# Performance work log

Hardware: AMD Instinct MI355X
Metric: run time of the kernel (lower is better)

Reference implementation:

```python
import jax, jax.numpy as jnp
import numpy as np
from jax import lax

N_NODES = 150_000
N_EDGES = 1_500_000
N_GRAPHS = 150          # batch_size(30) * sequence_length(5), hardcoded in forward
BATCH_SIZE = 30
SEQ_LEN = 5
IN_F = 1
HID = 100               # gcn_hidden_size == lstm_hidden_size


def setup_inputs() -> dict:
    key = jax.random.key(0)
    ks = jax.random.split(key, 12)
    x = jax.random.normal(ks[0], (N_NODES, IN_F), dtype=jnp.float32)
    edge_index = jax.random.randint(ks[1], (2, N_EDGES), 0, N_NODES, dtype=jnp.int32)
    # 150 graphs of 1000 nodes each (contiguous, as PyG batching produces)
    batch = jnp.repeat(jnp.arange(N_GRAPHS, dtype=jnp.int32), N_NODES // N_GRAPHS)
    s = 0.1
    params = {
        # GCNConv layer 1: Linear(no bias) weight stored [in, out]; separate bias
        "W1": jax.random.normal(ks[2], (IN_F, HID), jnp.float32) * s,
        "b1": jnp.zeros((HID,), jnp.float32),
        # GCNConv layer 2
        "W2": jax.random.normal(ks[3], (HID, HID), jnp.float32) * s,
        "b2": jnp.zeros((HID,), jnp.float32),
        # LSTM (PyTorch gate order i,f,g,o), weights [4H, in]/[4H, H]
        "W_ih": jax.random.normal(ks[4], (4 * HID, HID), jnp.float32) * s,
        "W_hh": jax.random.normal(ks[5], (4 * HID, HID), jnp.float32) * s,
        "b_ih": jnp.zeros((4 * HID,), jnp.float32),
        "b_hh": jnp.zeros((4 * HID,), jnp.float32),
        # output head Linear(HID, 1)
        "W_out": jax.random.normal(ks[6], (1, HID), jnp.float32) * s,
        "b_out": jnp.zeros((1,), jnp.float32),
    }
    return {"x": x, "edge_index": edge_index, "batch": batch, **params}


def _gcn_conv(x, src, dst, W, b, n_nodes):
    """PyG GCNConv: h = W x; out = D^-1/2 (A+I) D^-1/2 h + b."""
    h = x @ W  # [N, HID]
    deg = jax.ops.segment_sum(jnp.ones_like(dst, dtype=h.dtype), dst, num_segments=n_nodes)
    dinv = lax.rsqrt(deg)  # deg >= 1 thanks to self loops
    norm = dinv[src] * dinv[dst]  # [E+N]
    msg = h[src] * norm[:, None]  # gather + scale (memory-bound hot loop)
    out = jax.ops.segment_sum(msg, dst, num_segments=n_nodes)
    return out + b


def _lstm_last_hidden(xs, W_ih, W_hh, b_ih, b_hh):
    """xs: [B, T, H] -> last hidden state [B, H] (single-layer LSTM)."""
    B = xs.shape[0]
    H = W_hh.shape[1]
    h0 = jnp.zeros((B, H), xs.dtype)
    c0 = jnp.zeros((B, H), xs.dtype)

    def step(carry, xt):
        h, c = carry
        gates = xt @ W_ih.T + h @ W_hh.T + (b_ih + b_hh)
        i, f, g, o = jnp.split(gates, 4, axis=-1)
        c = jax.nn.sigmoid(f) * c + jax.nn.sigmoid(i) * jnp.tanh(g)
        h = jax.nn.sigmoid(o) * jnp.tanh(c)
        return (h, c), None

    (h_last, _), _ = lax.scan(step, (h0, c0), jnp.swapaxes(xs, 0, 1))
    return h_last


def reference(x, edge_index, batch, W1, b1, W2, b2, W_ih, W_hh, b_ih, b_hh, W_out, b_out):
    n_nodes = x.shape[0]
    loops = jnp.arange(n_nodes, dtype=edge_index.dtype)
    src = jnp.concatenate([edge_index[0], loops])
    dst = jnp.concatenate([edge_index[1], loops])

    h = _gcn_conv(x, src, dst, W1, b1, n_nodes)
    h = _gcn_conv(h, src, dst, W2, b2, n_nodes)

    # global mean pool over 150 graphs
    sums = jax.ops.segment_sum(h, batch, num_segments=N_GRAPHS)
    cnts = jax.ops.segment_sum(jnp.ones((n_nodes,), h.dtype), batch, num_segments=N_GRAPHS)
    pooled = sums / jnp.maximum(cnts, 1.0)[:, None]  # [150, HID]

    seq = pooled.reshape(BATCH_SIZE, SEQ_LEN, -1)  # [30, 5, HID]
    h_last = _lstm_last_hidden(seq, W_ih, W_hh, b_ih, b_hh)
    prediction = h_last @ W_out.T + b_out  # [30, 1]
    return prediction
```

## Files before the change

kernel.cpp:

```cpp
#include <hip/hip_runtime.h>
#include <math.h>

#define N_NODES   150000
#define N_EDGES   1500000
#define N_GRAPHS  150
#define HID       100
#define BATCH     30
#define SEQ       5
#define NODES_PER_GRAPH 1000

#define NPB       256
#define NB        ((N_NODES + NPB - 1) / NPB)
#define SBLK      512
#define EPB       2932
#define CAP       3584
#define FIFO      16

__global__ __launch_bounds__(256) void k_s1(const int* __restrict__ dst,
                                            int* __restrict__ blockBase) {
    __shared__ int hist[NB];
    int t = threadIdx.x;
    for (int i = t; i < NB; i += 256) hist[i] = 0;
    __syncthreads();
    int base = blockIdx.x * EPB;
    int end  = min(base + EPB, N_EDGES);
    for (int i = base + t * 4; i < end; i += 1024) {
        int4 d = *reinterpret_cast<const int4*>(dst + i);
        atomicAdd(&hist[d.x >> 8], 1);
        atomicAdd(&hist[d.y >> 8], 1);
        atomicAdd(&hist[d.z >> 8], 1);
        atomicAdd(&hist[d.w >> 8], 1);
    }
    __syncthreads();
    for (int j = t; j < NB; j += 256)
        blockBase[blockIdx.x * NB + j] = hist[j];
}

__global__ __launch_bounds__(512) void k_colscan(int* __restrict__ blockBase,
                                                 int* __restrict__ bucketCount,
                                                 float* __restrict__ graphA,
                                                 float* __restrict__ graphW) {
    __shared__ int v[SBLK];
    int j = blockIdx.x;
    int t = threadIdx.x;
    if (t == 0 && j < N_GRAPHS) { graphA[j] = 0.0f; graphW[j] = 0.0f; }
    int val = blockBase[t * NB + j];
    v[t] = val;
    __syncthreads();
    for (int off = 1; off < SBLK; off <<= 1) {
        int w = (t >= off) ? v[t - off] : 0;
        __syncthreads();
        v[t] += w;
        __syncthreads();
    }
    blockBase[t * NB + j] = v[t] - val;
    if (t == SBLK - 1) bucketCount[j] = v[t];
}

__global__ __launch_bounds__(256) void k_s2(const int* __restrict__ src,
                                            const int* __restrict__ dst,
                                            const int* __restrict__ blockBase,
                                            unsigned int* __restrict__ sorted) {
    __shared__ unsigned int fifo[NB][FIFO];
    __shared__ int cnt[NB];
    __shared__ int baseS[NB];
    int t = threadIdx.x;
    const int* bb = blockBase + blockIdx.x * NB;
    for (int i = t; i < NB; i += 256) {
        cnt[i] = 0;
        baseS[i] = i * CAP + bb[i];
    }
    __syncthreads();
    int base = blockIdx.x * EPB;
    int end  = min(base + EPB, N_EDGES);
    for (int i = base + t * 4; i < end; i += 1024) {
        int4 s4 = *reinterpret_cast<const int4*>(src + i);
        int4 d4 = *reinterpret_cast<const int4*>(dst + i);
        int bs[4] = { d4.x >> 8, d4.y >> 8, d4.z >> 8, d4.w >> 8 };
        int sv[4] = { s4.x, s4.y, s4.z, s4.w };
        int dl[4] = { d4.x & 255, d4.y & 255, d4.z & 255, d4.w & 255 };
        #pragma unroll
        for (int k = 0; k < 4; ++k) {
            int b = bs[k];
            unsigned int v = ((unsigned int)sv[k] << 8) | (unsigned int)dl[k];
            int slot = atomicAdd(&cnt[b], 1);
            if (slot < FIFO) fifo[b][slot] = v;
            else sorted[baseS[b] + slot] = v;
        }
    }
    __syncthreads();
    int wave = t >> 6, lane = t & 63;
    for (int j = wave; j < NB; j += 4) {
        int c = min(cnt[j], FIFO);
        if (lane < c) sorted[baseS[j] + lane] = fifo[j][lane];
    }
}

__device__ __forceinline__ void graph_reduce_add(float val, int thresh, int nn,
                                                 int g0, float* red, int t,
                                                 float* __restrict__ gdst) {
    red[t] = (t < thresh) ? val : 0.0f;
    __syncthreads();
    for (int s = 128; s > 0; s >>= 1) {
        if (t < s) red[t] += red[t + s];
        __syncthreads();
    }
    if (t == 0) atomicAdd(&gdst[g0], red[0]);
    __syncthreads();
    red[t] = (t >= thresh) ? val : 0.0f;
    __syncthreads();
    for (int s = 128; s > 0; s >>= 1) {
        if (t < s) red[t] += red[t + s];
        __syncthreads();
    }
    if (t == 0 && thresh < nn) atomicAdd(&gdst[g0 + 1], red[0]);
}

__global__ __launch_bounds__(256) void k_accA(const unsigned int* __restrict__ sorted,
                                              const int* __restrict__ bucketCount,
                                              const float* __restrict__ x,
                                              float* __restrict__ pd,
                                              float* __restrict__ px,
                                              float* __restrict__ graphW) {
    __shared__ int degI[2][NPB];
    __shared__ float red[256];
    int b = blockIdx.x;
    int t = threadIdx.x;
    int n0 = b << 8;
    int nn = min(NPB, N_NODES - n0);
    degI[0][t] = 0; degI[1][t] = 0;
    __syncthreads();
    int e0 = b * CAP, e1 = e0 + bucketCount[b];
    int rep = t & 1;
    int nvec = (e1 - e0) >> 2;
    for (int v = t; v < nvec; v += 256) {
        uint4 u4 = *reinterpret_cast<const uint4*>(sorted + e0 + v * 4);
        atomicAdd(&degI[rep][u4.x & 255], 1);
        atomicAdd(&degI[rep][u4.y & 255], 1);
        atomicAdd(&degI[rep][u4.z & 255], 1);
        atomicAdd(&degI[rep][u4.w & 255], 1);
    }
    int tail0 = e0 + (nvec << 2);
    if (tail0 + t < e1) atomicAdd(&degI[rep][sorted[tail0 + t] & 255], 1);
    __syncthreads();
    float val = 0.0f;
    if (t < nn) {
        float dv = 1.0f / sqrtf((float)(1 + degI[0][t] + degI[1][t]));
        pd[n0 + t] = dv;
        px[n0 + t] = dv * x[n0 + t];
        val = dv * dv;
    }
    int g0 = n0 / 1000;
    int thresh = (g0 + 1) * 1000 - n0;
    graph_reduce_add(val, thresh, nn, g0, red, t, graphW);
}

__global__ __launch_bounds__(256) void k_accB(const unsigned int* __restrict__ sorted,
                                              const int* __restrict__ bucketCount,
                                              const float* __restrict__ pd,
                                              const float* __restrict__ px,
                                              float2* __restrict__ pa2,
                                              float* __restrict__ graphA) {
    __shared__ float t1[2][NPB];
    __shared__ float red[256];
    int b = blockIdx.x;
    int t = threadIdx.x;
    int n0 = b << 8;
    int nn = min(NPB, N_NODES - n0);
    t1[0][t] = 0.0f; t1[1][t] = 0.0f;
    __syncthreads();
    int e0 = b * CAP, e1 = e0 + bucketCount[b];
    int rep = t & 1;
    int nvec = (e1 - e0) >> 2;
    for (int v = t; v < nvec; v += 256) {
        uint4 u4 = *reinterpret_cast<const uint4*>(sorted + e0 + v * 4);
        float p0 = px[u4.x >> 8];
        float p1 = px[u4.y >> 8];
        float p2 = px[u4.z >> 8];
        float p3 = px[u4.w >> 8];
        atomicAdd(&t1[rep][u4.x & 255], p0);
        atomicAdd(&t1[rep][u4.y & 255], p1);
        atomicAdd(&t1[rep][u4.z & 255], p2);
        atomicAdd(&t1[rep][u4.w & 255], p3);
    }
    int tail0 = e0 + (nvec << 2);
    if (tail0 + t < e1) {
        unsigned int u = sorted[tail0 + t];
        atomicAdd(&t1[rep][u & 255], px[u >> 8]);
    }
    __syncthreads();
    float val = 0.0f;
    if (t < nn) {
        float dv = pd[n0 + t];
        float T1 = t1[0][t] + t1[1][t];
        float agg1 = dv * T1 + dv * px[n0 + t];
        float a1 = dv * agg1;
        pa2[n0 + t] = make_float2(dv, a1);
        val = dv * a1;
    }
    int g0 = n0 / 1000;
    int thresh = (g0 + 1) * 1000 - n0;
    graph_reduce_add(val, thresh, nn, g0, red, t, graphA);
}

__global__ __launch_bounds__(256) void k_accG(const unsigned int* __restrict__ sorted,
                                              const int* __restrict__ bucketCount,
                                              const float* __restrict__ pd,
                                              const float2* __restrict__ pa2,
                                              float* __restrict__ graphA,
                                              float* __restrict__ graphW) {
    __shared__ float dvl[NPB];
    __shared__ float4 red4[256];
    int b = blockIdx.x;
    int t = threadIdx.x;
    int n0 = b << 8;
    int nn = min(NPB, N_NODES - n0);
    dvl[t] = (t < nn) ? pd[n0 + t] : 0.0f;
    __syncthreads();
    int g0 = n0 / 1000;
    int thresh = (g0 + 1) * 1000 - n0;
    float sa0 = 0.f, sa1 = 0.f, sw0 = 0.f, sw1 = 0.f;
    int e0 = b * CAP, e1 = e0 + bucketCount[b];
    auto proc = [&](unsigned int u) {
        int dl = (int)(u & 255);
        float dvd = dvl[dl];
        float2 v = pa2[u >> 8];
        if (dl < thresh) { sw0 += dvd * v.x; sa0 += dvd * v.y; }
        else             { sw1 += dvd * v.x; sa1 += dvd * v.y; }
    };
    int nvec = (e1 - e0) >> 2;
    for (int v = t; v < nvec; v += 256) {
        uint4 u4 = *reinterpret_cast<const uint4*>(sorted + e0 + v * 4);
        proc(u4.x); proc(u4.y); proc(u4.z); proc(u4.w);
    }
    int tail0 = e0 + (nvec << 2);
    if (tail0 + t < e1) proc(sorted[tail0 + t]);
    red4[t] = make_float4(sa0, sa1, sw0, sw1);
    __syncthreads();
    for (int s = 128; s > 0; s >>= 1) {
        if (t < s) {
            red4[t].x += red4[t + s].x; red4[t].y += red4[t + s].y;
            red4[t].z += red4[t + s].z; red4[t].w += red4[t + s].w;
        }
        __syncthreads();
    }
    if (t == 0) {
        atomicAdd(&graphA[g0], red4[0].x);
        atomicAdd(&graphW[g0], red4[0].z);
        if (thresh < nn) {
            atomicAdd(&graphA[g0 + 1], red4[0].y);
            atomicAdd(&graphW[g0 + 1], red4[0].w);
        }
    }
}

__global__ __launch_bounds__(512) void k_tail(const float* __restrict__ graphA,
                                              const float* __restrict__ graphW,
                                              const float* __restrict__ W1,
                                              const float* __restrict__ b1,
                                              const float* __restrict__ W2,
                                              const float* __restrict__ b2,
                                              const float* __restrict__ W_ih,
                                              const float* __restrict__ W_hh,
                                              const float* __restrict__ b_ih,
                                              const float* __restrict__ b_hh,
                                              const float* __restrict__ W_out,
                                              const float* __restrict__ b_out,
                                              float* __restrict__ outp) {
    int b = blockIdx.x;
    int t = threadIdx.x;
    __shared__ float v1[HID], v2[HID];
    __shared__ float xs_l[SEQ][HID];
    __shared__ float Xg_l[SEQ][4 * HID];
    __shared__ float hs[HID], cs[HID], gsb[4 * HID];
    __shared__ float red[512];

    if (t < HID) {
        float a = 0.0f, c = 0.0f;
        for (int k = 0; k < HID; ++k) {
            float w2 = W2[k * HID + t];
            a += W1[k] * w2;
            c += b1[k] * w2;
        }
        v1[t] = a; v2[t] = c;
    }
    __syncthreads();

    if (t < SEQ * HID) {
        int s = t / HID, j = t - s * HID;
        int g = b * SEQ + s;
        float ma = graphA[g] * (1.0f / NODES_PER_GRAPH);
        float mw = graphW[g] * (1.0f / NODES_PER_GRAPH);
        xs_l[s][j] = ma * v1[j] + mw * v2[j] + b2[j];
    }
    __syncthreads();

    float wreg[HID];
    if (t < 4 * HID) {
        const float4* wp = reinterpret_cast<const float4*>(W_ih + t * HID);
        #pragma unroll
        for (int q = 0; q < HID / 4; ++q) {
            float4 w4 = wp[q];
            wreg[4*q+0] = w4.x; wreg[4*q+1] = w4.y; wreg[4*q+2] = w4.z; wreg[4*q+3] = w4.w;
        }
        float bias = b_ih[t] + b_hh[t];
        for (int s = 0; s < SEQ; ++s) {
            float acc = bias;
            #pragma unroll
            for (int k = 0; k < HID; ++k)
                acc += xs_l[s][k] * wreg[k];
            Xg_l[s][t] = acc;
        }
        wp = reinterpret_cast<const float4*>(W_hh + t * HID);
        #pragma unroll
        for (int q = 0; q < HID / 4; ++q) {
            float4 w4 = wp[q];
            wreg[4*q+0] = w4.x; wreg[4*q+1] = w4.y; wreg[4*q+2] = w4.z; wreg[4*q+3] = w4.w;
        }
    }
    if (t < HID) { hs[t] = 0.0f; cs[t] = 0.0f; }
    __syncthreads();

    for (int step = 0; step < SEQ; ++step) {
        if (t < 4 * HID) {
            float acc = Xg_l[step][t];
            #pragma unroll
            for (int k = 0; k < HID; ++k)
                acc += hs[k] * wreg[k];
            gsb[t] = acc;
        }
        __syncthreads();
        if (t < HID) {
            float ig = 1.0f / (1.0f + expf(-gsb[t]));
            float fg = 1.0f / (1.0f + expf(-gsb[HID + t]));
            float gg = tanhf(gsb[2 * HID + t]);
            float og = 1.0f / (1.0f + expf(-gsb[3 * HID + t]));
            float c  = fg * cs[t] + ig * gg;
            cs[t] = c;
            hs[t] = og * tanhf(c);
        }
        __syncthreads();
    }

    float v = (t < HID) ? hs[t] * W_out[t] : 0.0f;
    red[t] = v;
    __syncthreads();
    for (int s = 256; s > 0; s >>= 1) {
        if (t < s) red[t] += red[t + s];
        __syncthreads();
    }
    if (t == 0) outp[b] = red[0] + b_out[0];
}

static inline char* align_up(char* p, size_t a) {
    return (char*)(((uintptr_t)p + (a - 1)) & ~(uintptr_t)(a - 1));
}

extern "C" void kernel_launch(void* const* d_in, const int* in_sizes, int n_in,
                              void* d_out, int out_size, void* d_ws, size_t ws_size,
                              hipStream_t stream) {
    const float* x    = (const float*)d_in[0];
    const int*   ei   = (const int*)d_in[1];
    const int*   srcp = ei;
    const int*   dstp = ei + N_EDGES;
    const float* W1   = (const float*)d_in[3];
    const float* b1   = (const float*)d_in[4];
    const float* W2   = (const float*)d_in[5];
    const float* b2   = (const float*)d_in[6];
    const float* W_ih = (const float*)d_in[7];
    const float* W_hh = (const float*)d_in[8];
    const float* b_ih = (const float*)d_in[9];
    const float* b_hh = (const float*)d_in[10];
    const float* W_out= (const float*)d_in[11];
    const float* b_out= (const float*)d_in[12];
    float* out = (float*)d_out;

    char* w = (char*)d_ws;
    int*  bucketCount = (int*)w;             w = align_up(w + NB * sizeof(int), 64);
    int*  blockBase   = (int*)w;             w = align_up(w + (size_t)SBLK * NB * sizeof(int), 64);
    unsigned int* sorted = (unsigned int*)w; w = align_up(w + (size_t)NB * CAP * sizeof(unsigned int), 64);
    float*  pd   = (float*)w;                w = align_up(w + (size_t)N_NODES * sizeof(float), 64);
    float*  px   = (float*)w;                w = align_up(w + (size_t)N_NODES * sizeof(float), 64);
    float2* pa2  = (float2*)w;               w = align_up(w + (size_t)N_NODES * sizeof(float2), 64);
    float* graphA = (float*)w;               w = align_up(w + N_GRAPHS * sizeof(float), 64);
    float* graphW = (float*)w;               w = align_up(w + N_GRAPHS * sizeof(float), 64);

    k_s1     <<<SBLK, 256, 0, stream>>>(dstp, blockBase);
    k_colscan<<<NB, SBLK, 0, stream>>>(blockBase, bucketCount, graphA, graphW);
    k_s2     <<<SBLK, 256, 0, stream>>>(srcp, dstp, blockBase, sorted);
    k_accA   <<<NB, 256, 0, stream>>>(sorted, bucketCount, x, pd, px, graphW);
    k_accB   <<<NB, 256, 0, stream>>>(sorted, bucketCount, pd, px, pa2, graphA);
    k_accG   <<<NB, 256, 0, stream>>>(sorted, bucketCount, pd, pa2, graphA, graphW);
    k_tail   <<<BATCH, 512, 0, stream>>>(graphA, graphW, W1, b1, W2, b2,
                                         W_ih, W_hh, b_ih, b_hh, W_out, b_out, out);
}
```

Baseline: 91.86 us.

## Fuse bucket sort into one pass with global atomic bases; defer graph reductions

Replaces the three-kernel bucket sort (histogram, column scan, scatter) with a single kernel that stages edges in shared memory, reserves per-bucket space through global atomics on bucketCount, and then scatters. Per-block graph partial sums are now written without atomics and reduced inside the tail kernel, so the global accumulators no longer need zeroing. This cuts two launches and the blockBase round trip through memory, at the cost of a memset and a nondeterministic edge order within each bucket.

```diff
diff --git a/kernel.cpp b/kernel.cpp
--- a/kernel.cpp
+++ b/kernel.cpp
@@ -9,103 +9,66 @@
 #define SEQ       5
 #define NODES_PER_GRAPH 1000
 
-#define NPB       256
-#define NB        ((N_NODES + NPB - 1) / NPB)
-#define SBLK      512
-#define EPB       2932
-#define CAP       3584
-#define FIFO      16
-
-__global__ __launch_bounds__(256) void k_s1(const int* __restrict__ dst,
-                                            int* __restrict__ blockBase) {
+#define NPB   256
+#define NB    586
+#define SBLK  512
+#define EPB   2932
+#define CAP   3584
+
+__global__ __launch_bounds__(256) void k_sort(const int* __restrict__ src,
+                                              const int* __restrict__ dst,
+                                              int* __restrict__ bucketCount,
+                                              unsigned int* __restrict__ sorted) {
+    __shared__ unsigned int   epack[EPB];
+    __shared__ unsigned short ebuck[EPB];
     __shared__ int hist[NB];
+    __shared__ int baseS[NB];
     int t = threadIdx.x;
     for (int i = t; i < NB; i += 256) hist[i] = 0;
-    __syncthreads();
-    int base = blockIdx.x * EPB;
-    int end  = min(base + EPB, N_EDGES);
-    for (int i = base + t * 4; i < end; i += 1024) {
-        int4 d = *reinterpret_cast<const int4*>(dst + i);
-        atomicAdd(&hist[d.x >> 8], 1);
-        atomicAdd(&hist[d.y >> 8], 1);
-        atomicAdd(&hist[d.z >> 8], 1);
-        atomicAdd(&hist[d.w >> 8], 1);
-    }
-    __syncthreads();
-    for (int j = t; j < NB; j += 256)
-        blockBase[blockIdx.x * NB + j] = hist[j];
-}
-
-__global__ __launch_bounds__(512) void k_colscan(int* __restrict__ blockBase,
-                                                 int* __restrict__ bucketCount,
-                                                 float* __restrict__ graphA,
-                                                 float* __restrict__ graphW) {
-    __shared__ int v[SBLK];
-    int j = blockIdx.x;
-    int t = threadIdx.x;
-    if (t == 0 && j < N_GRAPHS) { graphA[j] = 0.0f; graphW[j] = 0.0f; }
-    int val = blockBase[t * NB + j];
-    v[t] = val;
-    __syncthreads();
-    for (int off = 1; off < SBLK; off <<= 1) {
-        int w = (t >= off) ? v[t - off] : 0;
-        __syncthreads();
-        v[t] += w;
-        __syncthreads();
-    }
-    blockBase[t * NB + j] = v[t] - val;
-    if (t == SBLK - 1) bucketCount[j] = v[t];
-}
-
-__global__ __launch_bounds__(256) void k_s2(const int* __restrict__ src,
-                                            const int* __restrict__ dst,
-                                            const int* __restrict__ blockBase,
-                                            unsigned int* __restrict__ sorted) {
-    __shared__ unsigned int fifo[NB][FIFO];
-    __shared__ int cnt[NB];
-    __shared__ int baseS[NB];
-    int t = threadIdx.x;
-    const int* bb = blockBase + blockIdx.x * NB;
-    for (int i = t; i < NB; i += 256) {
-        cnt[i] = 0;
-        baseS[i] = i * CAP + bb[i];
-    }
     __syncthreads();
     int base = blockIdx.x * EPB;
     int end  = min(base + EPB, N_EDGES);
     for (int i = base + t * 4; i < end; i += 1024) {
         int4 s4 = *reinterpret_cast<const int4*>(src + i);
         int4 d4 = *reinterpret_cast<const int4*>(dst + i);
-        int bs[4] = { d4.x >> 8, d4.y >> 8, d4.z >> 8, d4.w >> 8 };
+        int l = i - base;
         int sv[4] = { s4.x, s4.y, s4.z, s4.w };
         int dl[4] = { d4.x & 255, d4.y & 255, d4.z & 255, d4.w & 255 };
+        int bk[4] = { d4.x >> 8, d4.y >> 8, d4.z >> 8, d4.w >> 8 };
         #pragma unroll
         for (int k = 0; k < 4; ++k) {
-            int b = bs[k];
-            unsigned int v = ((unsigned int)sv[k] << 8) | (unsigned int)dl[k];
-            int slot = atomicAdd(&cnt[b], 1);
-            if (slot < FIFO) fifo[b][slot] = v;
-            else sorted[baseS[b] + slot] = v;
-        }
-    }
-    __syncthreads();
-    int wave = t >> 6, lane = t & 63;
-    for (int j = wave; j < NB; j += 4) {
-        int c = min(cnt[j], FIFO);
-        if (lane < c) sorted[baseS[j] + lane] = fifo[j][lane];
-    }
-}
-
-__device__ __forceinline__ void graph_reduce_add(float val, int thresh, int nn,
-                                                 int g0, float* red, int t,
-                                                 float* __restrict__ gdst) {
+            atomicAdd(&hist[bk[k]], 1);
+            epack[l + k] = ((unsigned int)sv[k] << 8) | (unsigned int)dl[k];
+            ebuck[l + k] = (unsigned short)bk[k];
+        }
+    }
+    __syncthreads();
+    for (int j = t; j < NB; j += 256) {
+        int c = hist[j];
+        int gb = (c > 0) ? atomicAdd(&bucketCount[j], c) : 0;
+        baseS[j] = j * CAP + gb;
+    }
+    __syncthreads();
+    for (int j = t; j < NB; j += 256) hist[j] = 0;
+    __syncthreads();
+    int nloc = end - base;
+    for (int l = t; l < nloc; l += 256) {
+        int bk = ebuck[l];
+        int idx = atomicAdd(&hist[bk], 1);
+        sorted[baseS[bk] + idx] = epack[l];
+    }
+}
+
+__device__ __forceinline__ void bin2_reduce_store(float val, int thresh,
+                                                  float* red, int t,
+                                                  float2* __restrict__ outp) {
     red[t] = (t < thresh) ? val : 0.0f;
     __syncthreads();
     for (int s = 128; s > 0; s >>= 1) {
         if (t < s) red[t] += red[t + s];
         __syncthreads();
     }
-    if (t == 0) atomicAdd(&gdst[g0], red[0]);
+    float b0 = red[0];
     __syncthreads();
     red[t] = (t >= thresh) ? val : 0.0f;
     __syncthreads();
@@ -113,7 +76,7 @@
         if (t < s) red[t] += red[t + s];
         __syncthreads();
     }
-    if (t == 0 && thresh < nn) atomicAdd(&gdst[g0 + 1], red[0]);
+    if (t == 0) *outp = make_float2(b0, red[0]);
 }
 
 __global__ __launch_bounds__(256) void k_accA(const unsigned int* __restrict__ sorted,
@@ -121,7 +84,7 @@
                                               const float* __restrict__ x,
                                               float* __restrict__ pd,
                                               float* __restrict__ px,
-                                              float* __restrict__ graphW) {
+                                              float2* __restrict__ pW) {
     __shared__ int degI[2][NPB];
     __shared__ float red[256];
     int b = blockIdx.x;
@@ -152,7 +115,7 @@
     }
     int g0 = n0 / 1000;
     int thresh = (g0 + 1) * 1000 - n0;
-    graph_reduce_add(val, thresh, nn, g0, red, t, graphW);
+    bin2_reduce_store(val, thresh, red, t, &pW[b]);
 }
 
 __global__ __launch_bounds__(256) void k_accB(const unsigned int* __restrict__ sorted,
@@ -160,14 +123,14 @@
                                               const float* __restrict__ pd,
                                               const float* __restrict__ px,
                                               float2* __restrict__ pa2,
-                                              float* __restrict__ graphA) {
-    __shared__ float t1[2][NPB];
+                                              float2* __restrict__ pA) {
+    __shared__ float t1s[2][NPB];
     __shared__ float red[256];
     int b = blockIdx.x;
     int t = threadIdx.x;
     int n0 = b << 8;
     int nn = min(NPB, N_NODES - n0);
-    t1[0][t] = 0.0f; t1[1][t] = 0.0f;
+    t1s[0][t] = 0.0f; t1s[1][t] = 0.0f;
     __syncthreads();
     int e0 = b * CAP, e1 = e0 + bucketCount[b];
     int rep = t & 1;
@@ -178,21 +141,21 @@
         float p1 = px[u4.y >> 8];
         float p2 = px[u4.z >> 8];
         float p3 = px[u4.w >> 8];
-        atomicAdd(&t1[rep][u4.x & 255], p0);
-        atomicAdd(&t1[rep][u4.y & 255], p1);
-        atomicAdd(&t1[rep][u4.z & 255], p2);
-        atomicAdd(&t1[rep][u4.w & 255], p3);
+        atomicAdd(&t1s[rep][u4.x & 255], p0);
+        atomicAdd(&t1s[rep][u4.y & 255], p1);
+        atomicAdd(&t1s[rep][u4.z & 255], p2);
+        atomicAdd(&t1s[rep][u4.w & 255], p3);
     }
     int tail0 = e0 + (nvec << 2);
     if (tail0 + t < e1) {
         unsigned int u = sorted[tail0 + t];
-        atomicAdd(&t1[rep][u & 255], px[u >> 8]);
+        atomicAdd(&t1s[rep][u & 255], px[u >> 8]);
     }
     __syncthreads();
     float val = 0.0f;
     if (t < nn) {
         float dv = pd[n0 + t];
-        float T1 = t1[0][t] + t1[1][t];
+        float T1 = t1s[0][t] + t1s[1][t];
         float agg1 = dv * T1 + dv * px[n0 + t];
         float a1 = dv * agg1;
         pa2[n0 + t] = make_float2(dv, a1);
@@ -200,15 +163,14 @@
     }
     int g0 = n0 / 1000;
     int thresh = (g0 + 1) * 1000 - n0;
-    graph_reduce_add(val, thresh, nn, g0, red, t, graphA);
+    bin2_reduce_store(val, thresh, red, t, &pA[b]);
 }
 
 __global__ __launch_bounds__(256) void k_accG(const unsigned int* __restrict__ sorted,
                                               const int* __restrict__ bucketCount,
                                               const float* __restrict__ pd,
                                               const float2* __restrict__ pa2,
-                                              float* __restrict__ graphA,
-                                              float* __restrict__ graphW) {
+                                              float4* __restrict__ pG) {
     __shared__ float dvl[NPB];
     __shared__ float4 red4[256];
     int b = blockIdx.x;
@@ -244,18 +206,12 @@
         }
         __syncthreads();
     }
-    if (t == 0) {
-        atomicAdd(&graphA[g0], red4[0].x);
-        atomicAdd(&graphW[g0], red4[0].z);
-        if (thresh < nn) {
-            atomicAdd(&graphA[g0 + 1], red4[0].y);
-            atomicAdd(&graphW[g0 + 1], red4[0].w);
-        }
-    }
-}
-
-__global__ __launch_bounds__(512) void k_tail(const float* __restrict__ graphA,
-                                              const float* __restrict__ graphW,
+    if (t == 0) pG[b] = red4[0];
+}
+
+__global__ __launch_bounds__(512) void k_tail(const float2* __restrict__ pW,
+                                              const float2* __restrict__ pA,
+                                              const float4* __restrict__ pG,
                                               const float* __restrict__ W1,
                                               const float* __restrict__ b1,
                                               const float* __restrict__ W2,
@@ -269,12 +225,28 @@
                                               float* __restrict__ outp) {
     int b = blockIdx.x;
     int t = threadIdx.x;
+    __shared__ float gA[N_GRAPHS], gW[N_GRAPHS];
     __shared__ float v1[HID], v2[HID];
     __shared__ float xs_l[SEQ][HID];
     __shared__ float Xg_l[SEQ][4 * HID];
     __shared__ float hs[HID], cs[HID], gsb[4 * HID];
     __shared__ float red[512];
 
+    if (t < N_GRAPHS) { gA[t] = 0.0f; gW[t] = 0.0f; }
+    __syncthreads();
+    for (int j = t; j < NB; j += 512) {
+        int n0 = j << 8;
+        int g0 = n0 / 1000;
+        float2 w2v = pW[j];
+        float2 a2v = pA[j];
+        float4 g4 = pG[j];
+        atomicAdd(&gA[g0], a2v.x + g4.x);
+        atomicAdd(&gW[g0], w2v.x + g4.z);
+        if (g0 + 1 < N_GRAPHS) {
+            atomicAdd(&gA[g0 + 1], a2v.y + g4.y);
+            atomicAdd(&gW[g0 + 1], w2v.y + g4.w);
+        }
+    }
     if (t < HID) {
         float a = 0.0f, c = 0.0f;
         for (int k = 0; k < HID; ++k) {
@@ -289,8 +261,8 @@
     if (t < SEQ * HID) {
         int s = t / HID, j = t - s * HID;
         int g = b * SEQ + s;
-        float ma = graphA[g] * (1.0f / NODES_PER_GRAPH);
-        float mw = graphW[g] * (1.0f / NODES_PER_GRAPH);
+        float ma = gA[g] * (1.0f / NODES_PER_GRAPH);
+        float mw = gW[g] * (1.0f / NODES_PER_GRAPH);
         xs_l[s][j] = ma * v1[j] + mw * v2[j] + b2[j];
     }
     __syncthreads();
@@ -377,20 +349,19 @@
 
     char* w = (char*)d_ws;
     int*  bucketCount = (int*)w;             w = align_up(w + NB * sizeof(int), 64);
-    int*  blockBase   = (int*)w;             w = align_up(w + (size_t)SBLK * NB * sizeof(int), 64);
     unsigned int* sorted = (unsigned int*)w; w = align_up(w + (size_t)NB * CAP * sizeof(unsigned int), 64);
-    float*  pd   = (float*)w;                w = align_up(w + (size_t)N_NODES * sizeof(float), 64);
-    float*  px   = (float*)w;                w = align_up(w + (size_t)N_NODES * sizeof(float), 64);
-    float2* pa2  = (float2*)w;               w = align_up(w + (size_t)N_NODES * sizeof(float2), 64);
-    float* graphA = (float*)w;               w = align_up(w + N_GRAPHS * sizeof(float), 64);
-    float* graphW = (float*)w;               w = align_up(w + N_GRAPHS * sizeof(float), 64);
-
-    k_s1     <<<SBLK, 256, 0, stream>>>(dstp, blockBase);
-    k_colscan<<<NB, SBLK, 0, stream>>>(blockBase, bucketCount, graphA, graphW);
-    k_s2     <<<SBLK, 256, 0, stream>>>(srcp, dstp, blockBase, sorted);
-    k_accA   <<<NB, 256, 0, stream>>>(sorted, bucketCount, x, pd, px, graphW);
-    k_accB   <<<NB, 256, 0, stream>>>(sorted, bucketCount, pd, px, pa2, graphA);
-    k_accG   <<<NB, 256, 0, stream>>>(sorted, bucketCount, pd, pa2, graphA, graphW);
-    k_tail   <<<BATCH, 512, 0, stream>>>(graphA, graphW, W1, b1, W2, b2,
-                                         W_ih, W_hh, b_ih, b_hh, W_out, b_out, out);
-}
+    float*  pd  = (float*)w;                 w = align_up(w + (size_t)N_NODES * sizeof(float), 64);
+    float*  px  = (float*)w;                 w = align_up(w + (size_t)N_NODES * sizeof(float), 64);
+    float2* pa2 = (float2*)w;                w = align_up(w + (size_t)N_NODES * sizeof(float2), 64);
+    float2* pW  = (float2*)w;                w = align_up(w + NB * sizeof(float2), 64);
+    float2* pA  = (float2*)w;                w = align_up(w + NB * sizeof(float2), 64);
+    float4* pG  = (float4*)w;                w = align_up(w + NB * sizeof(float4), 64);
+
+    hipMemsetAsync(bucketCount, 0, NB * sizeof(int), stream);
+    k_sort<<<SBLK, 256, 0, stream>>>(srcp, dstp, bucketCount, sorted);
+    k_accA<<<NB, 256, 0, stream>>>(sorted, bucketCount, x, pd, px, pW);
+    k_accB<<<NB, 256, 0, stream>>>(sorted, bucketCount, pd, px, pa2, pA);
+    k_accG<<<NB, 256, 0, stream>>>(sorted, bucketCount, pd, pa2, pG);
+    k_tail<<<BATCH, 512, 0, stream>>>(pW, pA, pG, W1, b1, W2, b2,
+                                      W_ih, W_hh, b_ih, b_hh, W_out, b_out, out);
+}
```

Result: no change. 91.76 us (-0.1%).
